# Optimization experiments

Hardware: AMD Instinct MI355X
Metric: run time of the kernel (lower is better)

Reference implementation:

```python
import jax, jax.numpy as jnp
import numpy as np

S, B, D1, D2 = 256, 128, 1024, 1024
H1 = (D1 + D1) // 2  # 1024
H2 = (D1 + D2) // 2  # 1024


def setup_inputs() -> dict:
    key = jax.random.key(0)
    ks = jax.random.split(key, 11)
    s = lambda k, shp, fan_in: jax.random.normal(k, shp, jnp.float32) * (1.0 / np.sqrt(fan_in))
    return {
        "feature1": jax.random.normal(ks[0], (B, D1), jnp.float32),
        "feature2": jax.random.normal(ks[1], (B, D2), jnp.float32),
        "feature1_seq": jax.random.normal(ks[2], (S, B, D1), jnp.float32),
        "W11": s(ks[3], (2 * D1, H1), 2 * D1),
        "b11": jnp.zeros((H1,), jnp.float32),
        "W12": s(ks[4], (D1 + D2, H2), D1 + D2),
        "b12": jnp.zeros((H2,), jnp.float32),
        "W21": s(ks[5], (H1, 1), H1),
        "b21": jnp.zeros((1,), jnp.float32),
        "W22": s(ks[6], (H2, 1), H2),
        "b22": jnp.zeros((1,), jnp.float32),
    }


def reference(feature1, feature2, feature1_seq, W11, b11, W12, b12, W21, b21, W22, b22):
    # feature1_seq: [S, B, D1]; feature1: [B, D1]; feature2: [B, D2]
    seq_len = feature1_seq.shape[0]
    f1 = jnp.broadcast_to(feature1[None], (seq_len,) + feature1.shape)  # [S,B,D1]
    f2 = jnp.broadcast_to(feature2[None], (seq_len,) + feature2.shape)  # [S,B,D2]
    h1 = jnp.tanh(jnp.concatenate([feature1_seq, f1], axis=-1) @ W11 + b11)  # [S,B,H1]
    h2 = jnp.tanh(jnp.concatenate([feature1_seq, f2], axis=-1) @ W12 + b12)  # [S,B,H2]
    s1 = h1 @ W21 + b21  # [S,B,1]
    s2 = h2 @ W22 + b22  # [S,B,1]
    w1 = jax.nn.softmax(s1, axis=0)  # softmax over sequence dim
    w2 = jax.nn.softmax(s2, axis=0)
    # mean over sequence of (w1+w2)*seq/2 -> [B, D1]
    return jnp.mean((w1 + w2) * feature1_seq * 0.5, axis=0)
```

## Files before the change

### kernel.cpp

```cpp
#include <hip/hip_runtime.h>

#define S_LEN 256
#define B_SZ  128
#define M_ROWS (S_LEN * B_SZ)

typedef __attribute__((ext_vector_type(8))) short bf16x8;
typedef __attribute__((ext_vector_type(4))) float f32x4;

__device__ __forceinline__ unsigned short f2bf(float x) {
    unsigned u = __float_as_uint(x);
    unsigned r = (u + 0x7fffu + ((u >> 16) & 1u)) >> 16;
    return (unsigned short)r;
}

__device__ __forceinline__ void gl_lds16(const void* g, void* l) {
    __builtin_amdgcn_global_load_lds(
        (const __attribute__((address_space(1))) unsigned int*)g,
        (__attribute__((address_space(3))) unsigned int*)l,
        16, 0, 0);
}

__global__ __launch_bounds__(256) void convert_seq(const float* __restrict__ in,
                                                   unsigned short* __restrict__ out,
                                                   long n4) {
    long i = (long)blockIdx.x * blockDim.x + threadIdx.x;
    long stride = (long)gridDim.x * blockDim.x;
    for (; i < n4; i += stride) {
        float4 v = ((const float4*)in)[i];
        ushort4 o;
        o.x = f2bf(v.x); o.y = f2bf(v.y); o.z = f2bf(v.z); o.w = f2bf(v.w);
        ((ushort4*)out)[i] = o;
    }
}

__global__ __launch_bounds__(256) void convert_f(const float* __restrict__ f1,
                                                 const float* __restrict__ f2,
                                                 unsigned short* __restrict__ out) {
    int g = blockIdx.x * 256 + threadIdx.x;
    float4 v = (g < 32768) ? ((const float4*)f1)[g] : ((const float4*)f2)[g - 32768];
    ushort4 o;
    o.x = f2bf(v.x); o.y = f2bf(v.y); o.z = f2bf(v.z); o.w = f2bf(v.w);
    ((ushort4*)out)[g] = o;
}

__global__ __launch_bounds__(256) void transpose_w(const float* __restrict__ W11,
                                                   const float* __restrict__ W12,
                                                   unsigned short* __restrict__ Wt) {
    const int nt = blockIdx.x, kt = blockIdx.y, layer = blockIdx.z;
    const float* W = layer ? W12 : W11;
    __shared__ float T[64][65];
    const int c = threadIdx.x & 63, r4 = threadIdx.x >> 6;
    const int k0 = kt * 64, n0 = nt * 64;
    #pragma unroll
    for (int p = 0; p < 16; ++p) {
        int r = p * 4 + r4;
        T[r][c] = W[(size_t)(k0 + r) * 1024 + n0 + c];
    }
    __syncthreads();
    unsigned short* Wl = Wt + (size_t)layer * 1024 * 2048;
    #pragma unroll
    for (int p = 0; p < 16; ++p) {
        int n = p * 4 + r4;
        Wl[(size_t)(n0 + n) * 2048 + k0 + c] = f2bf(T[c][n]);
    }
}

__global__ __launch_bounds__(256) void c_precompute(const unsigned short* __restrict__ fbf,
                                                    const unsigned short* __restrict__ Wt,
                                                    const float* __restrict__ b11,
                                                    const float* __restrict__ b12,
                                                    float* __restrict__ cbuf) {
    __shared__ char smem[32768];
    unsigned short* ldsA = (unsigned short*)smem;
    unsigned short* ldsB = (unsigned short*)(smem + 16384);
    const int n0 = blockIdx.x * 128;
    const int layer = blockIdx.y;
    const int tid = threadIdx.x;
    const int w = tid >> 6, l = tid & 63;
    const int wm = w >> 1, wn = w & 1;
    const int lr = l & 15, lg = l >> 4;
    const unsigned short* Af = fbf + (size_t)layer * 128 * 1024;
    const unsigned short* Wl = Wt + (size_t)layer * 1024 * 2048;
    const float* bias = layer ? b12 : b11;

    f32x4 acc[4][4];
    #pragma unroll
    for (int i = 0; i < 4; ++i)
        #pragma unroll
        for (int j = 0; j < 4; ++j)
            #pragma unroll
            for (int e = 0; e < 4; ++e) acc[i][j][e] = 0.f;

    for (int kk = 0; kk < 1024; kk += 64) {
        __syncthreads();
        #pragma unroll
        for (int c = 0; c < 4; ++c) {
            int o = w * 4096 + c * 1024;
            int ob = o + l * 16;
            int row = ob >> 7, kb = ob & 127;
            gl_lds16((const char*)Af + ((size_t)row * 1024 + kk) * 2 + kb, (char*)ldsA + o);
            gl_lds16((const char*)Wl + ((size_t)(n0 + row) * 2048 + 1024 + kk) * 2 + kb, (char*)ldsB + o);
        }
        __syncthreads();
        #pragma unroll
        for (int ks = 0; ks < 2; ++ks) {
            bf16x8 av[4], bv[4];
            #pragma unroll
            for (int i = 0; i < 4; ++i) {
                av[i] = *(const bf16x8*)(ldsA + (wm * 64 + i * 16 + lr) * 64 + ks * 32 + lg * 8);
                bv[i] = *(const bf16x8*)(ldsB + (wn * 64 + i * 16 + lr) * 64 + ks * 32 + lg * 8);
            }
            #pragma unroll
            for (int i = 0; i < 4; ++i)
                #pragma unroll
                for (int j = 0; j < 4; ++j)
                    acc[i][j] = __builtin_amdgcn_mfma_f32_16x16x32_bf16(av[i], bv[j], acc[i][j], 0, 0, 0);
        }
    }
    float* cl = cbuf + (size_t)layer * 128 * 1024;
    #pragma unroll
    for (int i = 0; i < 4; ++i)
        #pragma unroll
        for (int j = 0; j < 4; ++j)
            #pragma unroll
            for (int q = 0; q < 4; ++q) {
                int rr = wm * 64 + i * 16 + lg * 4 + q;
                int hc = n0 + wn * 64 + j * 16 + lr;
                cl[(size_t)rr * 1024 + hc] = acc[i][j][q] + bias[hc];
            }
}


__global__ __launch_bounds__(512, 2) void fused_main(const unsigned short* __restrict__ Abf,
                                                     const unsigned short* __restrict__ Wt,
                                                     const float* __restrict__ cbuf,
                                                     const float* __restrict__ W21,
                                                     const float* __restrict__ W22,
                                                     float* __restrict__ sbufp) {
    __shared__ char smem[131072];
    const int bid = blockIdx.x;
    const int xcd = bid & 7;
    const int idx = bid >> 3;
    const int mtq = (idx & 3) + 4 * (idx >> 5);
    const int g   = (idx >> 2) & 7;
    const int mt  = xcd + 8 * mtq;
    const int layer = g >> 2;
    const int nt    = g & 3;
    const int n0 = nt * 256;

    const int tid = threadIdx.x;
    const int w = tid >> 6, l = tid & 63;
    const int wm = w >> 2, wn = w & 3;
    const int lr = l & 15, lg = l >> 4;

    const char* Ag = (const char*)Abf + (size_t)mt * 256 * 2048;
    const char* Bg = (const char*)(Wt + (size_t)layer * 1024 * 2048) + (size_t)n0 * 4096;

    const int dloc = tid * 16;
    const int gsw  = dloc ^ ((dloc >> 3) & 0x70);
    const int rowS = gsw >> 7, colS = gsw & 127;
    const char* srcA = Ag + (size_t)rowS * 2048 + colS;
    const char* srcB = Bg + (size_t)rowS * 4096 + colS;
    const int dstT = w * 1024;

    const int xr = (lr & 7) << 4;
    const int colx0 = (lg * 16) ^ xr;
    const int colx1 = (lg * 16 + 64) ^ xr;
    const int baseA = (wm * 128 + lr) * 128;
    const int baseB = 32768 + (wn * 64 + lr) * 128;

    f32x4 acc[8][4];
    #pragma unroll
    for (int i = 0; i < 8; ++i)
        #pragma unroll
        for (int j = 0; j < 4; ++j)
            #pragma unroll
            for (int e = 0; e < 4; ++e) acc[i][j][e] = 0.f;

    bf16x8 fA0[8], fA1[8], fB0[4], fB1[4];

#define STAGE(t) do {                                                   \
        char* d_ = smem + ((t) & 1) * 65536;                            \
        const char* a_ = srcA + (size_t)(t) * 128;                      \
        const char* b_ = srcB + (size_t)(t) * 128;                      \
        _Pragma("unroll")                                               \
        for (int r_ = 0; r_ < 4; ++r_) {                                \
            gl_lds16(a_ + r_ * 131072, d_ + r_ * 8192 + dstT);          \
            gl_lds16(b_ + r_ * 262144, d_ + 32768 + r_ * 8192 + dstT);  \
        }                                                               \
    } while (0)

#define LOADF(sA, sB, bo, cx) do {                                      \
        const char* ba_ = smem + (bo) + baseA;                          \
        const char* bb_ = smem + (bo) + baseB;                          \
        _Pragma("unroll")                                               \
        for (int i_ = 0; i_ < 8; ++i_) sA[i_] = *(const bf16x8*)(ba_ + i_ * 2048 + (cx)); \
        _Pragma("unroll")                                               \
        for (int j_ = 0; j_ < 4; ++j_) sB[j_] = *(const bf16x8*)(bb_ + j_ * 2048 + (cx)); \
    } while (0)

#define MF(sA, sB) do {                                                 \
        _Pragma("unroll")                                               \
        for (int i_ = 0; i_ < 8; ++i_)                                  \
            _Pragma("unroll")                                           \
            for (int j_ = 0; j_ < 4; ++j_)                              \
                acc[i_][j_] = __builtin_amdgcn_mfma_f32_16x16x32_bf16(  \
                    sA[i_], sB[j_], acc[i_][j_], 0, 0, 0);              \
    } while (0)

    STAGE(0);
    STAGE(1);
    __builtin_amdgcn_sched_barrier(0);
    asm volatile("s_waitcnt vmcnt(8)" ::: "memory");
    __builtin_amdgcn_sched_barrier(0);
    __builtin_amdgcn_s_barrier();
    __builtin_amdgcn_sched_barrier(0);
    LOADF(fA0, fB0, 0, colx0);

    for (int t = 0; t < 16; ++t) {
        const int bo = (t & 1) * 65536;
        LOADF(fA1, fB1, bo, colx1);
        MF(fA0, fB0);
        __builtin_amdgcn_sched_barrier(0);
        asm volatile("s_waitcnt lgkmcnt(0)" ::: "memory");
        asm volatile("s_waitcnt vmcnt(0)" ::: "memory");
        __builtin_amdgcn_sched_barrier(0);
        __builtin_amdgcn_s_barrier();
        __builtin_amdgcn_sched_barrier(0);
        if (t < 14) STAGE(t + 2);
        if (t < 15) LOADF(fA0, fB0, bo ^ 65536, colx0);
        MF(fA1, fB1);
        __builtin_amdgcn_sched_barrier(0);
    }

#undef STAGE
#undef LOADF
#undef MF

    __syncthreads();

    const float* cl = cbuf + (size_t)layer * 131072;
    const float* W2 = layer ? W22 : W21;
    float w2v[4];
    #pragma unroll
    for (int j = 0; j < 4; ++j) w2v[j] = W2[n0 + wn * 64 + j * 16 + lr];
    float* red = (float*)smem;
    #pragma unroll
    for (int i = 0; i < 8; ++i) {
        #pragma unroll
        for (int q = 0; q < 4; ++q) {
            int wrow = wm * 128 + i * 16 + lg * 4 + q;
            int brow = wrow & 127;
            float p = 0.f;
            #pragma unroll
            for (int j = 0; j < 4; ++j) {
                int col = n0 + wn * 64 + j * 16 + lr;
                float z = acc[i][j][q] + cl[(size_t)brow * 1024 + col];
                float e = __expf(2.f * z);
                p += (1.f - 2.f / (e + 1.f)) * w2v[j];
            }
            p += __shfl_xor(p, 1);
            p += __shfl_xor(p, 2);
            p += __shfl_xor(p, 4);
            p += __shfl_xor(p, 8);
            if (lr == 0) red[wrow * 4 + wn] = p;
        }
    }
    __syncthreads();
    if (tid < 256) {
        float v = red[tid * 4 + 0] + red[tid * 4 + 1] + red[tid * 4 + 2] + red[tid * 4 + 3];
        sbufp[(size_t)g * M_ROWS + (size_t)mt * 256 + tid] = v;
    }
}

__device__ __forceinline__ float block_max(float v, float* lds) {
    #pragma unroll
    for (int m = 32; m; m >>= 1) v = fmaxf(v, __shfl_xor(v, m));
    if ((threadIdx.x & 63) == 0) lds[threadIdx.x >> 6] = v;
    __syncthreads();
    v = fmaxf(fmaxf(lds[0], lds[1]), fmaxf(lds[2], lds[3]));
    __syncthreads();
    return v;
}
__device__ __forceinline__ float block_sum(float v, float* lds) {
    #pragma unroll
    for (int m = 32; m; m >>= 1) v += __shfl_xor(v, m);
    if ((threadIdx.x & 63) == 0) lds[threadIdx.x >> 6] = v;
    __syncthreads();
    v = lds[0] + lds[1] + lds[2] + lds[3];
    __syncthreads();
    return v;
}

__global__ __launch_bounds__(256) void coef_kernel(const float* __restrict__ sbufp,
                                                   float* __restrict__ coef,
                                                   float* __restrict__ out) {
    __shared__ float lds[4];
    const int b = blockIdx.x, s = threadIdx.x;
    float v1 = 0.f, v2 = 0.f;
    #pragma unroll
    for (int nt = 0; nt < 4; ++nt) {
        v1 += sbufp[(size_t)nt * M_ROWS + (size_t)s * 128 + b];
        v2 += sbufp[(size_t)(4 + nt) * M_ROWS + (size_t)s * 128 + b];
    }
    float m1 = block_max(v1, lds);
    float e1 = expf(v1 - m1);
    float S1 = block_sum(e1, lds);
    float m2 = block_max(v2, lds);
    float e2 = expf(v2 - m2);
    float S2 = block_sum(e2, lds);
    coef[(size_t)s * 128 + b] = (e1 / S1 + e2 / S2) * (0.5f / (float)S_LEN);
    float4 z4; z4.x = z4.y = z4.z = z4.w = 0.f;
    ((float4*)out)[(size_t)b * 256 + s] = z4;
}

__global__ __launch_bounds__(256) void final_kernel(const float* __restrict__ seq,
                                                    const float* __restrict__ coef,
                                                    float* __restrict__ out) {
    const int b = blockIdx.x, q = blockIdx.y;
    const int d0 = threadIdx.x * 4;
    float4 a; a.x = a.y = a.z = a.w = 0.f;
    for (int si = 0; si < 32; ++si) {
        int s = q * 32 + si;
        float cf = coef[(size_t)s * 128 + b];
        float4 v = *(const float4*)(seq + ((size_t)(s * 128 + b) * 1024 + d0));
        a.x += cf * v.x; a.y += cf * v.y; a.z += cf * v.z; a.w += cf * v.w;
    }
    float* o = out + (size_t)b * 1024 + d0;
    atomicAdd(o + 0, a.x);
    atomicAdd(o + 1, a.y);
    atomicAdd(o + 2, a.z);
    atomicAdd(o + 3, a.w);
}

extern "C" void kernel_launch(void* const* d_in, const int* in_sizes, int n_in,
                              void* d_out, int out_size, void* d_ws, size_t ws_size,
                              hipStream_t stream) {
    const float* feature1 = (const float*)d_in[0];
    const float* feature2 = (const float*)d_in[1];
    const float* seq      = (const float*)d_in[2];
    const float* W11      = (const float*)d_in[3];
    const float* b11      = (const float*)d_in[4];
    const float* W12      = (const float*)d_in[5];
    const float* b12      = (const float*)d_in[6];
    const float* W21      = (const float*)d_in[7];
    const float* W22      = (const float*)d_in[9];
    float* out = (float*)d_out;

    char* ws = (char*)d_ws;
    unsigned short* Abf   = (unsigned short*)(ws + 0);
    unsigned short* Wt    = (unsigned short*)(ws + 67108864);
    unsigned short* fbf   = (unsigned short*)(ws + 75497472);
    float*          cbuf  = (float*)(ws + 76021760);
    float*          sbufp = (float*)(ws + 77070336);
    float*          coef  = (float*)(ws + 78118912);

    convert_seq<<<2048, 256, 0, stream>>>(seq, Abf, (long)M_ROWS * 1024 / 4);
    convert_f<<<256, 256, 0, stream>>>(feature1, feature2, fbf);
    transpose_w<<<dim3(16, 32, 2), 256, 0, stream>>>(W11, W12, Wt);
    c_precompute<<<dim3(8, 2), 256, 0, stream>>>(fbf, Wt, b11, b12, cbuf);
    fused_main<<<1024, 512, 0, stream>>>(Abf, Wt, cbuf, W21, W22, sbufp);
    coef_kernel<<<128, 256, 0, stream>>>(sbufp, coef, out);
    final_kernel<<<dim3(128, 8), 256, 0, stream>>>(seq, coef, out);
}
```

Measured before the change: 262.0 us.

## Use 16-wave 64x64 warp tiles in fused GEMM and drop atomics in final reduction

```diff
diff --git a/kernel.cpp b/kernel.cpp
--- a/kernel.cpp
+++ b/kernel.cpp
@@ -131,12 +131,12 @@
 }
 
 
-__global__ __launch_bounds__(512, 2) void fused_main(const unsigned short* __restrict__ Abf,
-                                                     const unsigned short* __restrict__ Wt,
-                                                     const float* __restrict__ cbuf,
-                                                     const float* __restrict__ W21,
-                                                     const float* __restrict__ W22,
-                                                     float* __restrict__ sbufp) {
+__global__ __launch_bounds__(1024, 4) void fused_main(const unsigned short* __restrict__ Abf,
+                                                      const unsigned short* __restrict__ Wt,
+                                                      const float* __restrict__ cbuf,
+                                                      const float* __restrict__ W21,
+                                                      const float* __restrict__ W22,
+                                                      float* __restrict__ sbufp) {
     __shared__ char smem[131072];
     const int bid = blockIdx.x;
     const int xcd = bid & 7;
@@ -158,86 +158,81 @@
 
     const int dloc = tid * 16;
     const int gsw  = dloc ^ ((dloc >> 3) & 0x70);
-    const int rowS = gsw >> 7, colS = gsw & 127;
-    const char* srcA = Ag + (size_t)rowS * 2048 + colS;
-    const char* srcB = Bg + (size_t)rowS * 4096 + colS;
+    const char* srcA = Ag + (size_t)(gsw >> 7) * 2048 + (gsw & 127);
+    const char* srcB = Bg + (size_t)(gsw >> 7) * 4096 + (gsw & 127);
     const int dstT = w * 1024;
 
     const int xr = (lr & 7) << 4;
-    const int colx0 = (lg * 16) ^ xr;
-    const int colx1 = (lg * 16 + 64) ^ xr;
-    const int baseA = (wm * 128 + lr) * 128;
-    const int baseB = 32768 + (wn * 64 + lr) * 128;
-
-    f32x4 acc[8][4];
-    #pragma unroll
-    for (int i = 0; i < 8; ++i)
+    int offA[4], offB[4];
+    #pragma unroll
+    for (int i = 0; i < 4; ++i) {
+        offA[i] = (wm * 64 + i * 16 + lr) * 128 + ((lg * 16) ^ xr);
+        offB[i] = (wn * 64 + i * 16 + lr) * 128 + ((lg * 16) ^ xr);
+    }
+
+    f32x4 acc[4][4];
+    #pragma unroll
+    for (int i = 0; i < 4; ++i)
         #pragma unroll
         for (int j = 0; j < 4; ++j)
             #pragma unroll
             for (int e = 0; e < 4; ++e) acc[i][j][e] = 0.f;
 
-    bf16x8 fA0[8], fA1[8], fB0[4], fB1[4];
-
-#define STAGE(t) do {                                                   \
-        char* d_ = smem + ((t) & 1) * 65536;                            \
+#define STAGE(t, bi) do {                                               \
+        char* d_ = smem + (bi) * 65536;                                 \
         const char* a_ = srcA + (size_t)(t) * 128;                      \
         const char* b_ = srcB + (size_t)(t) * 128;                      \
+        gl_lds16(a_,              d_ +         dstT);                   \
+        gl_lds16(a_ + 128 * 2048, d_ + 16384 + dstT);                   \
+        gl_lds16(b_,              d_ + 32768 + dstT);                   \
+        gl_lds16(b_ + 128 * 4096, d_ + 49152 + dstT);                   \
+    } while (0)
+
+#define COMPUTE(bi) do {                                                \
+        const char* Ab_ = smem + (bi) * 65536;                          \
+        const char* Bb_ = Ab_ + 32768;                                  \
+        bf16x8 a0_[4], b0_[4], a1_[4], b1_[4];                          \
         _Pragma("unroll")                                               \
-        for (int r_ = 0; r_ < 4; ++r_) {                                \
-            gl_lds16(a_ + r_ * 131072, d_ + r_ * 8192 + dstT);          \
-            gl_lds16(b_ + r_ * 262144, d_ + 32768 + r_ * 8192 + dstT);  \
+        for (int i_ = 0; i_ < 4; ++i_) {                                \
+            a0_[i_] = *(const bf16x8*)(Ab_ + offA[i_]);                 \
+            b0_[i_] = *(const bf16x8*)(Bb_ + offB[i_]);                 \
+            a1_[i_] = *(const bf16x8*)(Ab_ + (offA[i_] ^ 64));          \
+            b1_[i_] = *(const bf16x8*)(Bb_ + (offB[i_] ^ 64));          \
         }                                                               \
-    } while (0)
-
-#define LOADF(sA, sB, bo, cx) do {                                      \
-        const char* ba_ = smem + (bo) + baseA;                          \
-        const char* bb_ = smem + (bo) + baseB;                          \
         _Pragma("unroll")                                               \
-        for (int i_ = 0; i_ < 8; ++i_) sA[i_] = *(const bf16x8*)(ba_ + i_ * 2048 + (cx)); \
-        _Pragma("unroll")                                               \
-        for (int j_ = 0; j_ < 4; ++j_) sB[j_] = *(const bf16x8*)(bb_ + j_ * 2048 + (cx)); \
-    } while (0)
-
-#define MF(sA, sB) do {                                                 \
-        _Pragma("unroll")                                               \
-        for (int i_ = 0; i_ < 8; ++i_)                                  \
+        for (int i_ = 0; i_ < 4; ++i_)                                  \
             _Pragma("unroll")                                           \
             for (int j_ = 0; j_ < 4; ++j_)                              \
                 acc[i_][j_] = __builtin_amdgcn_mfma_f32_16x16x32_bf16(  \
-                    sA[i_], sB[j_], acc[i_][j_], 0, 0, 0);              \
+                    a0_[i_], b0_[j_], acc[i_][j_], 0, 0, 0);            \
+        _Pragma("unroll")                                               \
+        for (int i_ = 0; i_ < 4; ++i_)                                  \
+            _Pragma("unroll")                                           \
+            for (int j_ = 0; j_ < 4; ++j_)                              \
+                acc[i_][j_] = __builtin_amdgcn_mfma_f32_16x16x32_bf16(  \
+                    a1_[i_], b1_[j_], acc[i_][j_], 0, 0, 0);            \
     } while (0)
 
-    STAGE(0);
-    STAGE(1);
+    STAGE(0, 0);
     __builtin_amdgcn_sched_barrier(0);
-    asm volatile("s_waitcnt vmcnt(8)" ::: "memory");
+    asm volatile("s_waitcnt vmcnt(0)" ::: "memory");
     __builtin_amdgcn_sched_barrier(0);
     __builtin_amdgcn_s_barrier();
     __builtin_amdgcn_sched_barrier(0);
-    LOADF(fA0, fB0, 0, colx0);
 
     for (int t = 0; t < 16; ++t) {
-        const int bo = (t & 1) * 65536;
-        LOADF(fA1, fB1, bo, colx1);
-        MF(fA0, fB0);
+        const int cur = t & 1;
+        if (t < 15) STAGE(t + 1, cur ^ 1);
+        COMPUTE(cur);
         __builtin_amdgcn_sched_barrier(0);
-        asm volatile("s_waitcnt lgkmcnt(0)" ::: "memory");
         asm volatile("s_waitcnt vmcnt(0)" ::: "memory");
         __builtin_amdgcn_sched_barrier(0);
         __builtin_amdgcn_s_barrier();
         __builtin_amdgcn_sched_barrier(0);
-        if (t < 14) STAGE(t + 2);
-        if (t < 15) LOADF(fA0, fB0, bo ^ 65536, colx0);
-        MF(fA1, fB1);
-        __builtin_amdgcn_sched_barrier(0);
     }
 
 #undef STAGE
-#undef LOADF
-#undef MF
-
-    __syncthreads();
+#undef COMPUTE
 
     const float* cl = cbuf + (size_t)layer * 131072;
     const float* W2 = layer ? W22 : W21;
@@ -246,10 +241,10 @@
     for (int j = 0; j < 4; ++j) w2v[j] = W2[n0 + wn * 64 + j * 16 + lr];
     float* red = (float*)smem;
     #pragma unroll
-    for (int i = 0; i < 8; ++i) {
+    for (int i = 0; i < 4; ++i) {
         #pragma unroll
         for (int q = 0; q < 4; ++q) {
-            int wrow = wm * 128 + i * 16 + lg * 4 + q;
+            int wrow = wm * 64 + i * 16 + lg * 4 + q;
             int brow = wrow & 127;
             float p = 0.f;
             #pragma unroll
@@ -293,8 +288,7 @@
 }
 
 __global__ __launch_bounds__(256) void coef_kernel(const float* __restrict__ sbufp,
-                                                   float* __restrict__ coef,
-                                                   float* __restrict__ out) {
+                                                   float* __restrict__ coef) {
     __shared__ float lds[4];
     const int b = blockIdx.x, s = threadIdx.x;
     float v1 = 0.f, v2 = 0.f;
@@ -310,27 +304,19 @@
     float e2 = expf(v2 - m2);
     float S2 = block_sum(e2, lds);
     coef[(size_t)s * 128 + b] = (e1 / S1 + e2 / S2) * (0.5f / (float)S_LEN);
-    float4 z4; z4.x = z4.y = z4.z = z4.w = 0.f;
-    ((float4*)out)[(size_t)b * 256 + s] = z4;
 }
 
 __global__ __launch_bounds__(256) void final_kernel(const float* __restrict__ seq,
                                                     const float* __restrict__ coef,
                                                     float* __restrict__ out) {
-    const int b = blockIdx.x, q = blockIdx.y;
-    const int d0 = threadIdx.x * 4;
-    float4 a; a.x = a.y = a.z = a.w = 0.f;
-    for (int si = 0; si < 32; ++si) {
-        int s = q * 32 + si;
-        float cf = coef[(size_t)s * 128 + b];
-        float4 v = *(const float4*)(seq + ((size_t)(s * 128 + b) * 1024 + d0));
-        a.x += cf * v.x; a.y += cf * v.y; a.z += cf * v.z; a.w += cf * v.w;
-    }
-    float* o = out + (size_t)b * 1024 + d0;
-    atomicAdd(o + 0, a.x);
-    atomicAdd(o + 1, a.y);
-    atomicAdd(o + 2, a.z);
-    atomicAdd(o + 3, a.w);
+    const int b = blockIdx.x, dq = blockIdx.y;
+    const int d = dq * 256 + threadIdx.x;
+    float a = 0.f;
+    #pragma unroll 8
+    for (int s = 0; s < 256; ++s) {
+        a += coef[(size_t)s * 128 + b] * seq[(size_t)(s * 128 + b) * 1024 + d];
+    }
+    out[(size_t)b * 1024 + d] = a;
 }
 
 extern "C" void kernel_launch(void* const* d_in, const int* in_sizes, int n_in,
@@ -359,7 +345,7 @@
     convert_f<<<256, 256, 0, stream>>>(feature1, feature2, fbf);
     transpose_w<<<dim3(16, 32, 2), 256, 0, stream>>>(W11, W12, Wt);
     c_precompute<<<dim3(8, 2), 256, 0, stream>>>(fbf, Wt, b11, b12, cbuf);
-    fused_main<<<1024, 512, 0, stream>>>(Abf, Wt, cbuf, W21, W22, sbufp);
-    coef_kernel<<<128, 256, 0, stream>>>(sbufp, coef, out);
-    final_kernel<<<dim3(128, 8), 256, 0, stream>>>(seq, coef, out);
-}
+    fused_main<<<1024, 1024, 0, stream>>>(Abf, Wt, cbuf, W21, W22, sbufp);
+    coef_kernel<<<128, 256, 0, stream>>>(sbufp, coef);
+    final_kernel<<<dim3(128, 4), 256, 0, stream>>>(seq, coef, out);
+}
```

New measurement: 231.8 us. 1.13x faster.
